# Performance work log

Hardware: AMD Instinct MI355X
Metric: run time of the kernel (lower is better)

Reference implementation:

```python
import jax, jax.numpy as jnp
import numpy as np

N_NODES = 10000
N_EDGES = 640000
IN_CH = 128
HID = 128
OUT = 2


def setup_inputs() -> dict:
    key = jax.random.key(0)
    ks = jax.random.split(key, 12)
    s_in = 1.0 / np.sqrt(IN_CH)
    s_2h = 1.0 / np.sqrt(2 * HID)
    s_h = 1.0 / np.sqrt(HID)
    return {
        "x": jax.random.normal(ks[0], (N_NODES, IN_CH), dtype=jnp.float32),
        "edge_index": jax.random.randint(ks[1], (2, N_EDGES), 0, N_NODES, dtype=jnp.int64),
        # SAGEConv: lin_l applied to aggregated neighbors (has bias), lin_r to self (no bias)
        "W_l": jax.random.uniform(ks[2], (IN_CH, HID), jnp.float32, -s_in, s_in),
        "b_l": jax.random.uniform(ks[3], (HID,), jnp.float32, -s_in, s_in),
        "W_r": jax.random.uniform(ks[4], (IN_CH, HID), jnp.float32, -s_in, s_in),
        # lin0: in -> hid
        "W0": jax.random.uniform(ks[5], (IN_CH, HID), jnp.float32, -s_in, s_in),
        "b0": jax.random.uniform(ks[6], (HID,), jnp.float32, -s_in, s_in),
        # lin1: 2*hid -> hid
        "W1": jax.random.uniform(ks[7], (2 * HID, HID), jnp.float32, -s_2h, s_2h),
        "b1": jax.random.uniform(ks[8], (HID,), jnp.float32, -s_2h, s_2h),
        # lin2: hid -> out
        "W2": jax.random.uniform(ks[9], (HID, OUT), jnp.float32, -s_h, s_h),
        "b2": jax.random.uniform(ks[10], (OUT,), jnp.float32, -s_h, s_h),
    }


def reference(x, edge_index, W_l, b_l, W_r, W0, b0, W1, b1, W2, b2):
    src, dst = edge_index[0], edge_index[1]
    # SAGE mean aggregation: gather source features, scatter-mean onto dst nodes
    msgs = x[src]                                                # [E, in]
    agg = jax.ops.segment_sum(msgs, dst, num_segments=N_NODES)  # [N, in]
    deg = jax.ops.segment_sum(jnp.ones((src.shape[0],), x.dtype), dst,
                              num_segments=N_NODES)              # [N]
    agg = agg / jnp.maximum(deg, 1.0)[:, None]
    # SAGEConv output: lin_l(agg) + lin_r(x)
    h = agg @ W_l + b_l + x @ W_r                                # [N, hid]
    h = jax.nn.relu(h)
    h = jnp.max(h, axis=-2)                                      # [hid] global max pool over nodes
    # concat branch: news node is x[0]
    news = jax.nn.relu(x[0] @ W0 + b0)                           # [hid]
    h = jax.nn.relu(jnp.concatenate([news, h], axis=-1) @ W1 + b1)
    return h @ W2 + b2                                           # [out]
```

## Files before the change

kernel.cpp:

```cpp
#include <hip/hip_runtime.h>
#include <hip/hip_bf16.h>

#define NCH 128
#define NPART 256
#define NRANGE 512
#define SEGCAP 24
#define SEGSTR 32
#define RCAP 2560
#define PSMAX 32

typedef __attribute__((ext_vector_type(8))) short bfrag;
typedef __attribute__((ext_vector_type(4))) float ffrag;
typedef __attribute__((ext_vector_type(2))) float f32x2;

__device__ inline unsigned int f2bf_pair(float lo, float hi) {
    unsigned int ul = __float_as_uint(lo);
    unsigned int uh = __float_as_uint(hi);
    ul = (ul + 0x7fffu + ((ul >> 16) & 1u)) >> 16;
    uh = (uh + 0x7fffu + ((uh >> 16) & 1u)) & 0xffff0000u;
    return (ul & 0xffffu) | uh;
}

__device__ inline void gchunk16(const unsigned short* scsr, int base, int i,
                                const unsigned int* __restrict__ xqU, int lq,
                                int half, float& a0, float& a1, float& a2,
                                float& a3) {
    int s[16]; unsigned int u[16];
#pragma unroll
    for (int j = 0; j < 16; ++j) s[j] = scsr[base + i + 2 * j + half];
#pragma unroll
    for (int j = 0; j < 16; ++j) u[j] = xqU[s[j] * 32 + lq];
#pragma unroll
    for (int j = 0; j < 16; ++j) {
        f32x2 v0 = __builtin_amdgcn_cvt_pk_f32_fp8(u[j], false);
        f32x2 v1 = __builtin_amdgcn_cvt_pk_f32_fp8(u[j], true);
        a0 += v0.x; a1 += v0.y; a2 += v1.x; a3 += v1.y;
    }
}

__device__ inline void gchunk16x2(const unsigned short* scsr, int b1, int i1,
                                  int b2, int i2,
                                  const unsigned int* __restrict__ xqU, int lq,
                                  int half, float& p0, float& p1, float& p2,
                                  float& p3, float& q0, float& q1, float& q2,
                                  float& q3) {
    int sA[16], sB[16]; unsigned int uA[16], uB[16];
#pragma unroll
    for (int j = 0; j < 16; ++j) sA[j] = scsr[b1 + i1 + 2 * j + half];
#pragma unroll
    for (int j = 0; j < 16; ++j) sB[j] = scsr[b2 + i2 + 2 * j + half];
#pragma unroll
    for (int j = 0; j < 16; ++j) uA[j] = xqU[sA[j] * 32 + lq];
#pragma unroll
    for (int j = 0; j < 16; ++j) uB[j] = xqU[sB[j] * 32 + lq];
#pragma unroll
    for (int j = 0; j < 16; ++j) {
        f32x2 v0 = __builtin_amdgcn_cvt_pk_f32_fp8(uA[j], false);
        f32x2 v1 = __builtin_amdgcn_cvt_pk_f32_fp8(uA[j], true);
        p0 += v0.x; p1 += v0.y; p2 += v1.x; p3 += v1.y;
        f32x2 w0 = __builtin_amdgcn_cvt_pk_f32_fp8(uB[j], false);
        f32x2 w1 = __builtin_amdgcn_cvt_pk_f32_fp8(uB[j], true);
        q0 += w0.x; q1 += w0.y; q2 += w1.x; q3 += w1.y;
    }
}

__device__ inline void gtail(const unsigned short* scsr, int base, int i, int d,
                             const unsigned int* __restrict__ xqU, int lq,
                             int half, float& a0, float& a1, float& a2,
                             float& a3) {
    int s[16]; unsigned int u[16];
#pragma unroll
    for (int j = 0; j < 16; ++j) {
        int idx = i + 2 * j + half;
        s[j] = scsr[base + min(idx, d - 1)];
    }
#pragma unroll
    for (int j = 0; j < 16; ++j) u[j] = xqU[s[j] * 32 + lq];
#pragma unroll
    for (int j = 0; j < 16; ++j) {
        int idx = i + 2 * j + half;
        if (idx < d) {
            f32x2 v0 = __builtin_amdgcn_cvt_pk_f32_fp8(u[j], false);
            f32x2 v1 = __builtin_amdgcn_cvt_pk_f32_fp8(u[j], true);
            a0 += v0.x; a1 += v0.y; a2 += v1.x; a3 += v1.y;
        }
    }
}

__global__ __launch_bounds__(512) void k_partprep(
    const float4* __restrict__ x4, const float* __restrict__ Wl,
    const float* __restrict__ Wr, const int* __restrict__ ei32,
    const long long* __restrict__ ei64, unsigned int* __restrict__ M32,
    unsigned int* __restrict__ Wt32, unsigned int* __restrict__ xqU,
    unsigned int* __restrict__ seg, unsigned int* __restrict__ hmaxU,
    int* __restrict__ done, int nq, int N, int E, int PSr, unsigned int Mdiv) {
    const int t = threadIdx.x;
    if (blockIdx.x < NPART) {
        if (blockIdx.x == 0) {
            if (t < 128) hmaxU[t] = 0u;
            if (t == 128) *done = 0;
        }
        __shared__ int sflag;
        __shared__ int cur[NRANGE];
        if (t < 64) {
            int v = ei32[2 * t + 1];
            unsigned long long b = __ballot(v != 0);
            if (t == 0) sflag = (b == 0ULL) ? 1 : 0;
        }
        for (int i = t; i < NRANGE; i += 512) cur[i] = 0;
        __syncthreads();
        const int flag = sflag;
        const int b = blockIdx.x;
        const int ES = (E + NPART - 1) / NPART;
        const int e0 = b * ES, e1 = min(E, e0 + ES);
        for (int bb = e0; bb < e1; bb += 2048) {
            int ebase = bb + t * 4;
            int m = min(4, e1 - ebase);
            if (m <= 0) continue;
            int src4[4], dst4[4];
            if (m == 4) {
                if (flag) {
                    const int4* ps = (const int4*)(ei64 + ebase);
                    const int4* pd = (const int4*)(ei64 + (size_t)E + ebase);
                    int4 q0 = ps[0], q1 = ps[1];
                    int4 r0 = pd[0], r1 = pd[1];
                    src4[0] = q0.x; src4[1] = q0.z; src4[2] = q1.x; src4[3] = q1.z;
                    dst4[0] = r0.x; dst4[1] = r0.z; dst4[2] = r1.x; dst4[3] = r1.z;
                } else {
                    int4 q = *(const int4*)(ei32 + ebase);
                    int4 r0 = *(const int4*)(ei32 + (size_t)E + ebase);
                    src4[0] = q.x; src4[1] = q.y; src4[2] = q.z; src4[3] = q.w;
                    dst4[0] = r0.x; dst4[1] = r0.y; dst4[2] = r0.z; dst4[3] = r0.w;
                }
            } else {
#pragma unroll
                for (int j = 0; j < 4; ++j) {
                    if (j < m) {
                        if (flag) {
                            src4[j] = (int)ei64[ebase + j];
                            dst4[j] = (int)ei64[(size_t)E + ebase + j];
                        } else {
                            src4[j] = ei32[ebase + j];
                            dst4[j] = ei32[(size_t)E + ebase + j];
                        }
                    }
                }
            }
#pragma unroll
            for (int j = 0; j < 4; ++j) {
                if (j < m) {
                    int dstj = dst4[j];
                    int r = Mdiv ? (int)__umulhi((unsigned int)dstj, Mdiv) : dstj;
                    int dl = dstj - r * PSr;
                    int pos = atomicAdd(&cur[r], 1);
                    if (pos < SEGCAP)
                        seg[((size_t)b * NRANGE + r) * SEGSTR + 1 + pos] =
                            ((unsigned int)dl << 16) | (unsigned int)src4[j];
                }
            }
        }
        __syncthreads();
        for (int i = t; i < NRANGE; i += 512)
            seg[((size_t)b * NRANGE + i) * SEGSTR] =
                (unsigned int)min(cur[i], SEGCAP);
        return;
    }
    int i = (int)(blockIdx.x - NPART) * 512 + t;
    if (i < nq) {
        float4 v = x4[i];
        int n = i >> 5, cq = i & 31;
        unsigned int p0 = f2bf_pair(v.x, v.y);
        unsigned int p1 = f2bf_pair(v.z, v.w);
        *(uint2*)(M32 + (size_t)n * 128 + 64 + 2 * cq) = make_uint2(p0, p1);
        unsigned int q = __builtin_amdgcn_cvt_pk_fp8_f32(v.x, v.y, 0u, false);
        q = __builtin_amdgcn_cvt_pk_fp8_f32(v.z, v.w, q, true);
        xqU[(size_t)n * 32 + cq] = q;
        return;
    }
    int j = i - nq;
    if (j < 128 * 128) {
        int c = j & 127, kp = j >> 7;
        int k0 = 2 * kp, k1 = 2 * kp + 1;
        float v0 = (k0 < 128) ? Wl[k0 * 128 + c] : Wr[(k0 - 128) * 128 + c];
        float v1 = (k1 < 128) ? Wl[k1 * 128 + c] : Wr[(k1 - 128) * 128 + c];
        Wt32[c * 128 + kp] = f2bf_pair(v0, v1);
    }
}

__global__ __launch_bounds__(512) void k_aggdense(
    const unsigned int* __restrict__ seg, const unsigned int* __restrict__ M32,
    const unsigned short* __restrict__ xq, const short* __restrict__ Wt,
    const float* __restrict__ bl, unsigned int* __restrict__ hmaxU,
    int* __restrict__ done, const float* __restrict__ x,
    const float* __restrict__ W0, const float* __restrict__ b0,
    const float* __restrict__ W1, const float* __restrict__ b1,
    const float* __restrict__ W2, const float* __restrict__ b2,
    float* __restrict__ out, int N, int PSr) {
    __shared__ unsigned short scsr[RCAP];
    __shared__ unsigned int aggL[PSMAX * 66];
    __shared__ int hist[PSMAX], startp[PSMAX], cur[PSMAX];
    __shared__ float red[8][32];
    __shared__ float hs[1280];
    __shared__ int lastflag;
    const int r = blockIdx.x;
    const int t = threadIdx.x;
    const int wave = t >> 6, lane = t & 63;

    int mycnt = 0;
    uint4 e0 = make_uint4(0, 0, 0, 0), e1 = make_uint4(0, 0, 0, 0),
          e2 = make_uint4(0, 0, 0, 0), e3 = make_uint4(0, 0, 0, 0),
          e4 = make_uint4(0, 0, 0, 0), e5 = make_uint4(0, 0, 0, 0),
          e6 = make_uint4(0, 0, 0, 0);
    if (t < NPART) {
        const uint4* sp = (const uint4*)(seg + ((size_t)t * NRANGE + r) * SEGSTR);
        e0 = sp[0]; e1 = sp[1];
        mycnt = min((int)e0.x, SEGCAP);
        if (mycnt > 7)  e2 = sp[2];
        if (mycnt > 11) e3 = sp[3];
        if (mycnt > 15) e4 = sp[4];
        if (mycnt > 19) e5 = sp[5];
        if (mycnt > 23) e6 = sp[6];
    }

    for (int i = t; i < PSMAX * 66; i += 512) aggL[i] = 0;
    if (t < PSMAX) hist[t] = 0;
    __syncthreads();

#define HIST4(ev, kk)                                                          \
    {                                                                          \
        if ((kk) * 4 + 0 >= 1 && (kk) * 4 + 0 <= mycnt)                        \
            atomicAdd(&hist[(ev).x >> 16], 1);                                 \
        if ((kk) * 4 + 1 <= mycnt) atomicAdd(&hist[(ev).y >> 16], 1);          \
        if ((kk) * 4 + 2 <= mycnt) atomicAdd(&hist[(ev).z >> 16], 1);          \
        if ((kk) * 4 + 3 <= mycnt) atomicAdd(&hist[(ev).w >> 16], 1);          \
    }
    HIST4(e0, 0) HIST4(e1, 1) HIST4(e2, 2) HIST4(e3, 3)
    HIST4(e4, 4) HIST4(e5, 5) HIST4(e6, 6)
#undef HIST4
    __syncthreads();
    if (t < PSMAX) {
        int h = hist[t];
        int ip = h;
#pragma unroll
        for (int off = 1; off < PSMAX; off <<= 1) {
            int u = __shfl_up(ip, off);
            if (lane >= off) ip += u;
        }
        startp[t] = ip - h;
        cur[t] = ip - h;
    }
    __syncthreads();
#define SCAT4(ev, kk)                                                          \
    {                                                                          \
        if ((kk) * 4 + 0 >= 1 && (kk) * 4 + 0 <= mycnt) {                      \
            int p_ = atomicAdd(&cur[(ev).x >> 16], 1);                         \
            if (p_ < RCAP) scsr[p_] = (unsigned short)((ev).x & 0xffffu);      \
        }                                                                      \
        if ((kk) * 4 + 1 <= mycnt) {                                           \
            int p_ = atomicAdd(&cur[(ev).y >> 16], 1);                         \
            if (p_ < RCAP) scsr[p_] = (unsigned short)((ev).y & 0xffffu);      \
        }                                                                      \
        if ((kk) * 4 + 2 <= mycnt) {                                           \
            int p_ = atomicAdd(&cur[(ev).z >> 16], 1);                         \
            if (p_ < RCAP) scsr[p_] = (unsigned short)((ev).z & 0xffffu);      \
        }                                                                      \
        if ((kk) * 4 + 3 <= mycnt) {                                           \
            int p_ = atomicAdd(&cur[(ev).w >> 16], 1);                         \
            if (p_ < RCAP) scsr[p_] = (unsigned short)((ev).w & 0xffffu);      \
        }                                                                      \
    }
    SCAT4(e0, 0) SCAT4(e1, 1) SCAT4(e2, 2) SCAT4(e3, 3)
    SCAT4(e4, 4) SCAT4(e5, 5) SCAT4(e6, 6)
#undef SCAT4
    __syncthreads();

    const int l16 = lane & 15, quad = lane >> 4;
    const int rt = wave & 1, cg = wave >> 1;
    const int lrow = rt * 16 + l16;
    bfrag a[8];
    {
        int mc = min(r * PSr + lrow, N - 1);
#pragma unroll
        for (int kk = 0; kk < 4; ++kk)
            a[4 + kk] = *(const bfrag*)((const short*)(M32 + (size_t)mc * 128 + 64)
                                        + kk * 32 + quad * 8);
    }

    const unsigned int* __restrict__ xqU = (const unsigned int*)xq;
    const int half = lane >> 5, lq = lane & 31;
    const int H = (PSr + 1) >> 1;
    for (int li = wave; li < H; li += 8) {
        int n1 = r * PSr + li;
        if (n1 >= N) break;
        int lj = li + H;
        bool v2 = (lj < PSr) && (r * PSr + lj < N);
        int b1 = startp[li], d1 = hist[li];
        int b2 = v2 ? startp[lj] : 0, d2 = v2 ? hist[lj] : 0;
        float p0 = 0.f, p1 = 0.f, p2 = 0.f, p3 = 0.f;
        float q0 = 0.f, q1 = 0.f, q2 = 0.f, q3 = 0.f;
        int i1 = 0, i2 = 0;
        for (; i1 + 32 <= d1 && i2 + 32 <= d2; i1 += 32, i2 += 32)
            gchunk16x2(scsr, b1, i1, b2, i2, xqU, lq, half,
                       p0, p1, p2, p3, q0, q1, q2, q3);
        for (; i1 + 32 <= d1; i1 += 32)
            gchunk16(scsr, b1, i1, xqU, lq, half, p0, p1, p2, p3);
        for (; i2 + 32 <= d2; i2 += 32)
            gchunk16(scsr, b2, i2, xqU, lq, half, q0, q1, q2, q3);
        if (i1 < d1) gtail(scsr, b1, i1, d1, xqU, lq, half, p0, p1, p2, p3);
        if (i2 < d2) gtail(scsr, b2, i2, d2, xqU, lq, half, q0, q1, q2, q3);
        p0 += __shfl_xor(p0, 32); p1 += __shfl_xor(p1, 32);
        p2 += __shfl_xor(p2, 32); p3 += __shfl_xor(p3, 32);
        q0 += __shfl_xor(q0, 32); q1 += __shfl_xor(q1, 32);
        q2 += __shfl_xor(q2, 32); q3 += __shfl_xor(q3, 32);
        float s1 = 1.0f / fmaxf((float)d1, 1.0f);
        float s2 = 1.0f / fmaxf((float)d2, 1.0f);
        if (half == 0) {
            aggL[li * 66 + 2 * lq]     = f2bf_pair(p0 * s1, p1 * s1);
            aggL[li * 66 + 2 * lq + 1] = f2bf_pair(p2 * s1, p3 * s1);
            if (v2) {
                aggL[lj * 66 + 2 * lq]     = f2bf_pair(q0 * s2, q1 * s2);
                aggL[lj * 66 + 2 * lq + 1] = f2bf_pair(q2 * s2, q3 * s2);
            }
        }
    }
    __syncthreads();

#pragma unroll
    for (int kk = 0; kk < 4; ++kk)
        a[kk] = *(const bfrag*)((const short*)(aggL + lrow * 66 + kk * 16 + quad * 4));
    float mx[2];
#pragma unroll
    for (int ct = 0; ct < 2; ++ct) {
        int col = cg * 32 + ct * 16 + l16;
        float bv = bl[col];
        ffrag acc = {bv, bv, bv, bv};
        const short* wp = Wt + (size_t)col * 256 + quad * 8;
#pragma unroll
        for (int kk = 0; kk < 8; ++kk) {
            bfrag b = *(const bfrag*)(wp + kk * 32);
            acc = __builtin_amdgcn_mfma_f32_16x16x32_bf16(a[kk], b, acc, 0, 0, 0);
        }
        float lm = 0.f;
#pragma unroll
        for (int rr = 0; rr < 4; ++rr) {
            int lr = rt * 16 + quad * 4 + rr;
            int nd = r * PSr + lr;
            if (lr < PSr && nd < N) lm = fmaxf(lm, fmaxf(acc[rr], 0.f));
        }
        lm = fmaxf(lm, __shfl_xor(lm, 16));
        lm = fmaxf(lm, __shfl_xor(lm, 32));
        mx[ct] = lm;
    }
    if (lane < 16) {
        red[wave][l16]      = mx[0];
        red[wave][16 + l16] = mx[1];
    }
    __syncthreads();
    if (t < 128) {
        int cg2 = t >> 5, wi = t & 31;
        float v = fmaxf(red[2 * cg2][wi], red[2 * cg2 + 1][wi]);
        atomicMax(&hmaxU[t], __float_as_uint(v));
    }

    __syncthreads();
    if (t == 0) {
        __threadfence();
        int old = atomicAdd(done, 1);
        lastflag = (old == NRANGE - 1) ? 1 : 0;
    }
    __syncthreads();
    if (!lastflag) return;
    __threadfence();

    float* cat  = hs;
    float* part = hs + 256;
    float* h1p  = hs + 768;
    float* pr   = hs + 896;
    float* xsp  = hs + 1152;
    const int c = t & 127, sg = t >> 7;
    if (t < 128) {
        xsp[t] = x[t];
        cat[128 + t] = __uint_as_float(atomicOr(&hmaxU[t], 0u));
    }
    __syncthreads();
    {
        float a0 = 0.f, a1 = 0.f, a2 = 0.f, a3 = 0.f;
        int k0 = sg * 32;
#pragma unroll
        for (int j = 0; j < 32; j += 4) {
            a0 += xsp[k0 + j + 0] * W0[(k0 + j + 0) * NCH + c];
            a1 += xsp[k0 + j + 1] * W0[(k0 + j + 1) * NCH + c];
            a2 += xsp[k0 + j + 2] * W0[(k0 + j + 2) * NCH + c];
            a3 += xsp[k0 + j + 3] * W0[(k0 + j + 3) * NCH + c];
        }
        part[sg * 128 + c] = (a0 + a1) + (a2 + a3);
    }
    __syncthreads();
    if (t < 128)
        cat[t] = fmaxf(b0[t] + part[t] + part[128 + t] + part[256 + t] + part[384 + t], 0.f);
    __syncthreads();
    {
        float a0 = 0.f, a1 = 0.f, a2 = 0.f, a3 = 0.f;
        int k0 = sg * 64;
#pragma unroll
        for (int j = 0; j < 64; j += 4) {
            a0 += cat[k0 + j + 0] * W1[(k0 + j + 0) * NCH + c];
            a1 += cat[k0 + j + 1] * W1[(k0 + j + 1) * NCH + c];
            a2 += cat[k0 + j + 2] * W1[(k0 + j + 2) * NCH + c];
            a3 += cat[k0 + j + 3] * W1[(k0 + j + 3) * NCH + c];
        }
        part[sg * 128 + c] = (a0 + a1) + (a2 + a3);
    }
    __syncthreads();
    if (t < 128)
        h1p[t] = fmaxf(b1[t] + part[t] + part[128 + t] + part[256 + t] + part[384 + t], 0.f);
    __syncthreads();
    if (t < 128) {
        float2 w = ((const float2*)W2)[t];
        pr[t]       = h1p[t] * w.x;
        pr[128 + t] = h1p[t] * w.y;
    }
    __syncthreads();
    for (int off = 64; off >= 1; off >>= 1) {
        if (t < off) { pr[t] += pr[t + off]; pr[128 + t] += pr[128 + t + off]; }
        __syncthreads();
    }
    if (t == 0) out[0] = pr[0] + b2[0];
    if (t == 1) out[1] = pr[128] + b2[1];
}

__global__ void k_detect(const int* __restrict__ ei, int* __restrict__ flag) {
    int v = ei[2 * threadIdx.x + 1];
    unsigned long long b = __ballot(v != 0);
    if (threadIdx.x == 0) *flag = (b == 0ULL) ? 1 : 0;
}
__global__ void k_hist(const int* __restrict__ ei32, const long long* __restrict__ ei64,
                       const int* __restrict__ flag, int* __restrict__ cnt, int E) {
    int e = blockIdx.x * blockDim.x + threadIdx.x;
    if (e >= E) return;
    int dst = (*flag) ? (int)ei64[(size_t)E + e] : ei32[(size_t)E + e];
    atomicAdd(&cnt[dst], 1);
}
__global__ void k_scan(const int* __restrict__ cnt, int* __restrict__ row_start, int N) {
    __shared__ int lds[1024];
    int t = threadIdx.x;
    int chunk = (N + 1023) / 1024;
    int base = t * chunk;
    int sum = 0;
    for (int i = 0; i < chunk; ++i) {
        int idx = base + i;
        if (idx < N) sum += cnt[idx];
    }
    lds[t] = sum;
    __syncthreads();
    for (int off = 1; off < 1024; off <<= 1) {
        int v = (t >= off) ? lds[t - off] : 0;
        __syncthreads();
        lds[t] += v;
        __syncthreads();
    }
    int run = (t == 0) ? 0 : lds[t - 1];
    for (int i = 0; i < chunk; ++i) {
        int idx = base + i;
        if (idx < N) { row_start[idx] = run; run += cnt[idx]; }
    }
    if (t == 1023) row_start[N] = run;
}
__global__ void k_fill(const int* __restrict__ ei32, const long long* __restrict__ ei64,
                       const int* __restrict__ flag, const int* __restrict__ row_start,
                       int* __restrict__ cursor, int* __restrict__ csr, int E) {
    int e = blockIdx.x * blockDim.x + threadIdx.x;
    if (e >= E) return;
    int src, dst;
    if (*flag) { src = (int)ei64[e]; dst = (int)ei64[(size_t)E + e]; }
    else       { src = ei32[e];      dst = ei32[(size_t)E + e]; }
    int pos = atomicAdd(&cursor[dst], 1);
    csr[row_start[dst] + pos] = src;
}
__global__ __launch_bounds__(256) void k_agg_linmax(
    const float* __restrict__ x, const int* __restrict__ row_start,
    const int* __restrict__ csr, const float* __restrict__ Wl,
    const float* __restrict__ bl, const float* __restrict__ Wr,
    unsigned int* __restrict__ hmaxU, int N, int E) {
    const int lane = threadIdx.x & 63;
    const int wave = threadIdx.x >> 6;
    const int group = blockIdx.x * 4 + wave;
    const int ngroups = (N + 3) / 4;
    const float2* __restrict__ x2  = (const float2*)x;
    const float2* __restrict__ Wl2 = (const float2*)Wl;
    const float2* __restrict__ Wr2 = (const float2*)Wr;
    const float2* __restrict__ bl2 = (const float2*)bl;
    float2 m = make_float2(0.f, 0.f);
    if (group < ngroups) {
        int n0 = group * 4;
        int s[4], d[4];
#pragma unroll
        for (int q = 0; q < 4; ++q) {
            int n = n0 + q;
            if (n < N) { s[q] = row_start[n]; d[q] = row_start[n + 1] - s[q]; }
            else       { s[q] = 0; d[q] = 0; }
        }
        int maxd = max(max(d[0], d[1]), max(d[2], d[3]));
        float2 acc[4];
#pragma unroll
        for (int q = 0; q < 4; ++q) acc[q] = make_float2(0.f, 0.f);
        int idxv[4] = {0, 0, 0, 0};
        for (int i = 0; i < maxd; ++i) {
            int t = i & 63;
            if (t == 0) {
#pragma unroll
                for (int q = 0; q < 4; ++q) {
                    if (i < d[q]) {
                        int a = s[q] + i + lane;
                        a = (a < E) ? a : (E - 1);
                        idxv[q] = csr[a];
                    }
                }
            }
#pragma unroll
            for (int q = 0; q < 4; ++q) {
                if (i < d[q]) {
                    int src = __shfl(idxv[q], t);
                    float2 v = x2[src * 64 + lane];
                    acc[q].x += v.x; acc[q].y += v.y;
                }
            }
        }
        float2 xv[4];
#pragma unroll
        for (int q = 0; q < 4; ++q) {
            float sc = 1.0f / fmaxf((float)d[q], 1.0f);
            acc[q].x *= sc; acc[q].y *= sc;
            int n = n0 + q;
            xv[q] = (n < N) ? x2[n * 64 + lane] : make_float2(0.f, 0.f);
        }
        float2 o[4];
#pragma unroll
        for (int q = 0; q < 4; ++q) o[q] = bl2[lane];
        for (int j = 0; j < 64; ++j) {
            float2 wl0 = Wl2[(2 * j) * 64 + lane];
            float2 wl1 = Wl2[(2 * j + 1) * 64 + lane];
            float2 wr0 = Wr2[(2 * j) * 64 + lane];
            float2 wr1 = Wr2[(2 * j + 1) * 64 + lane];
#pragma unroll
            for (int q = 0; q < 4; ++q) {
                float ax = __shfl(acc[q].x, j);
                float ay = __shfl(acc[q].y, j);
                float xx = __shfl(xv[q].x, j);
                float xy = __shfl(xv[q].y, j);
                o[q].x += ax * wl0.x + ay * wl1.x + xx * wr0.x + xy * wr1.x;
                o[q].y += ax * wl0.y + ay * wl1.y + xx * wr0.y + xy * wr1.y;
            }
        }
#pragma unroll
        for (int q = 0; q < 4; ++q) {
            if (n0 + q < N) {
                m.x = fmaxf(m.x, fmaxf(o[q].x, 0.f));
                m.y = fmaxf(m.y, fmaxf(o[q].y, 0.f));
            }
        }
    }
    __shared__ float2 red2[4][64];
    red2[wave][lane] = m;
    __syncthreads();
    if (wave == 0) {
#pragma unroll
        for (int ww = 1; ww < 4; ++ww) {
            m.x = fmaxf(m.x, red2[ww][lane].x);
            m.y = fmaxf(m.y, red2[ww][lane].y);
        }
        atomicMax(&hmaxU[2 * lane],     __float_as_uint(m.x));
        atomicMax(&hmaxU[2 * lane + 1], __float_as_uint(m.y));
    }
}
__global__ void k_head_fb(const float* __restrict__ x, const float* __restrict__ hmax,
                          const float* __restrict__ W0, const float* __restrict__ b0,
                          const float* __restrict__ W1, const float* __restrict__ b1,
                          const float* __restrict__ W2, const float* __restrict__ b2,
                          float* __restrict__ out) {
    __shared__ float s_cat[2 * NCH];
    __shared__ float s_part[256];
    __shared__ float s_h1[NCH];
    int t = threadIdx.x;
    if (t < NCH) {
        float acc = b0[t];
        for (int k = 0; k < NCH; ++k) acc += x[k] * W0[k * NCH + t];
        s_cat[t] = fmaxf(acc, 0.f);
        s_cat[NCH + t] = hmax[t];
    }
    __syncthreads();
    {
        int c = t & 127, half = t >> 7;
        float p = 0.f;
        int k0 = half * NCH;
        for (int k = k0; k < k0 + NCH; ++k) p += s_cat[k] * W1[k * NCH + c];
        s_part[t] = p;
    }
    __syncthreads();
    if (t < NCH) s_h1[t] = fmaxf(s_part[t] + s_part[NCH + t] + b1[t], 0.f);
    __syncthreads();
    if (t < 2) {
        float o = b2[t];
        for (int k = 0; k < NCH; ++k) o += s_h1[k] * W2[k * 2 + t];
        out[t] = o;
    }
}

extern "C" void kernel_launch(void* const* d_in, const int* in_sizes, int n_in,
                              void* d_out, int out_size, void* d_ws, size_t ws_size,
                              hipStream_t stream) {
    const float* x  = (const float*)d_in[0];
    const void*  ei = d_in[1];
    const float* Wl = (const float*)d_in[2];
    const float* bl = (const float*)d_in[3];
    const float* Wr = (const float*)d_in[4];
    const float* W0 = (const float*)d_in[5];
    const float* b0 = (const float*)d_in[6];
    const float* W1 = (const float*)d_in[7];
    const float* b1 = (const float*)d_in[8];
    const float* W2 = (const float*)d_in[9];
    const float* b2 = (const float*)d_in[10];
    float* out = (float*)d_out;

    const int N = in_sizes[0] / NCH;
    const int E = in_sizes[1] / 2;
    const int nq = N * 32;
    const int PSr = (N + NRANGE - 1) / NRANGE;

    int* iws = (int*)d_ws;
    unsigned int* hmaxU = (unsigned int*)iws;
    int* done = iws + 128;
    unsigned int* seg = (unsigned int*)(iws + 192);
    unsigned int* Wt32 = seg + (size_t)NPART * NRANGE * SEGSTR;
    unsigned int* M32  = Wt32 + 128 * 128;
    unsigned short* xq = (unsigned short*)(M32 + (size_t)N * 128);
    size_t need = ((size_t)192 + (size_t)NPART * NRANGE * SEGSTR + 128 * 128 +
                   (size_t)N * 128 + (size_t)N * 32) * 4;
    bool main_ok = (need <= ws_size) && (N <= NRANGE * PSMAX) && (N <= 65535) &&
                   (PSr >= 1) && (PSr <= PSMAX);

    if (main_ok) {
        unsigned int Mdiv = (PSr > 1)
            ? (unsigned int)(0x100000000ULL / (unsigned long long)PSr + 1ULL)
            : 0u;
        int prepb = (nq + 128 * 128 + 511) / 512;
        k_partprep<<<NPART + prepb, 512, 0, stream>>>(
            (const float4*)x, Wl, Wr, (const int*)ei, (const long long*)ei,
            M32, Wt32, (unsigned int*)xq, seg, hmaxU, done, nq, N, E,
            PSr, Mdiv);
        k_aggdense<<<NRANGE, 512, 0, stream>>>(seg, M32, xq,
                                               (const short*)Wt32,
                                               bl, hmaxU, done, x,
                                               W0, b0, W1, b1, W2, b2, out, N, PSr);
        return;
    }

    int* fcnt      = iws;
    int* fcursor   = iws + N;
    unsigned int* fhmax = (unsigned int*)(iws + 2 * N);
    int* flag      = iws + 2 * N + 128;
    int* frs       = iws + 2 * N + 132;
    int* fcsr      = iws + 3 * N + 144;

    hipMemsetAsync(d_ws, 0, (size_t)(2 * N + 128) * sizeof(int), stream);
    k_detect<<<1, 64, 0, stream>>>((const int*)ei, flag);
    k_hist<<<(E + 255) / 256, 256, 0, stream>>>((const int*)ei, (const long long*)ei,
                                                flag, fcnt, E);
    k_scan<<<1, 1024, 0, stream>>>(fcnt, frs, N);
    k_fill<<<(E + 255) / 256, 256, 0, stream>>>((const int*)ei, (const long long*)ei,
                                                flag, frs, fcursor, fcsr, E);
    int ngroups = (N + 3) / 4;
    k_agg_linmax<<<(ngroups + 3) / 4, 256, 0, stream>>>(x, frs, fcsr, Wl, bl, Wr,
                                                        fhmax, N, E);
    k_head_fb<<<1, 256, 0, stream>>>(x, (const float*)fhmax, W0, b0, W1, b1, W2, b2, out);
}
```

Baseline: 129.3 us.

## Replace atomic last-block reduction with separate head kernel and transpose segment layout

Replaces the global atomicMax plus done-counter last-block pattern with a per-block colmax array and a separate single-block head kernel that reduces it and runs the MLP. Transposes the segment buffer layout so each aggregation block reads contiguous per-range data. Loads the first four segment vectors unconditionally, and drops the two-node-interleaved gather in favour of a simpler one-node-per-wave loop. This trades an extra kernel launch and a colmax round trip for removing threadfence/atomic serialisation, but may lose the memory-level parallelism of the paired gathers.

New measurement: 133.2 us. +3.0%, slower.

```diff
diff --git a/kernel.cpp b/kernel.cpp
--- a/kernel.cpp
+++ b/kernel.cpp
@@ -38,32 +38,6 @@
     }
 }
 
-__device__ inline void gchunk16x2(const unsigned short* scsr, int b1, int i1,
-                                  int b2, int i2,
-                                  const unsigned int* __restrict__ xqU, int lq,
-                                  int half, float& p0, float& p1, float& p2,
-                                  float& p3, float& q0, float& q1, float& q2,
-                                  float& q3) {
-    int sA[16], sB[16]; unsigned int uA[16], uB[16];
-#pragma unroll
-    for (int j = 0; j < 16; ++j) sA[j] = scsr[b1 + i1 + 2 * j + half];
-#pragma unroll
-    for (int j = 0; j < 16; ++j) sB[j] = scsr[b2 + i2 + 2 * j + half];
-#pragma unroll
-    for (int j = 0; j < 16; ++j) uA[j] = xqU[sA[j] * 32 + lq];
-#pragma unroll
-    for (int j = 0; j < 16; ++j) uB[j] = xqU[sB[j] * 32 + lq];
-#pragma unroll
-    for (int j = 0; j < 16; ++j) {
-        f32x2 v0 = __builtin_amdgcn_cvt_pk_f32_fp8(uA[j], false);
-        f32x2 v1 = __builtin_amdgcn_cvt_pk_f32_fp8(uA[j], true);
-        p0 += v0.x; p1 += v0.y; p2 += v1.x; p3 += v1.y;
-        f32x2 w0 = __builtin_amdgcn_cvt_pk_f32_fp8(uB[j], false);
-        f32x2 w1 = __builtin_amdgcn_cvt_pk_f32_fp8(uB[j], true);
-        q0 += w0.x; q1 += w0.y; q2 += w1.x; q3 += w1.y;
-    }
-}
-
 __device__ inline void gtail(const unsigned short* scsr, int base, int i, int d,
                              const unsigned int* __restrict__ xqU, int lq,
                              int half, float& a0, float& a1, float& a2,
@@ -92,14 +66,10 @@
     const float* __restrict__ Wr, const int* __restrict__ ei32,
     const long long* __restrict__ ei64, unsigned int* __restrict__ M32,
     unsigned int* __restrict__ Wt32, unsigned int* __restrict__ xqU,
-    unsigned int* __restrict__ seg, unsigned int* __restrict__ hmaxU,
-    int* __restrict__ done, int nq, int N, int E, int PSr, unsigned int Mdiv) {
+    unsigned int* __restrict__ seg, int nq, int N, int E, int PSr,
+    unsigned int Mdiv) {
     const int t = threadIdx.x;
     if (blockIdx.x < NPART) {
-        if (blockIdx.x == 0) {
-            if (t < 128) hmaxU[t] = 0u;
-            if (t == 128) *done = 0;
-        }
         __shared__ int sflag;
         __shared__ int cur[NRANGE];
         if (t < 64) {
@@ -154,14 +124,14 @@
                     int dl = dstj - r * PSr;
                     int pos = atomicAdd(&cur[r], 1);
                     if (pos < SEGCAP)
-                        seg[((size_t)b * NRANGE + r) * SEGSTR + 1 + pos] =
+                        seg[((size_t)r * NPART + b) * SEGSTR + 1 + pos] =
                             ((unsigned int)dl << 16) | (unsigned int)src4[j];
                 }
             }
         }
         __syncthreads();
         for (int i = t; i < NRANGE; i += 512)
-            seg[((size_t)b * NRANGE + i) * SEGSTR] =
+            seg[((size_t)i * NPART + b) * SEGSTR] =
                 (unsigned int)min(cur[i], SEGCAP);
         return;
     }
@@ -190,18 +160,11 @@
 __global__ __launch_bounds__(512) void k_aggdense(
     const unsigned int* __restrict__ seg, const unsigned int* __restrict__ M32,
     const unsigned short* __restrict__ xq, const short* __restrict__ Wt,
-    const float* __restrict__ bl, unsigned int* __restrict__ hmaxU,
-    int* __restrict__ done, const float* __restrict__ x,
-    const float* __restrict__ W0, const float* __restrict__ b0,
-    const float* __restrict__ W1, const float* __restrict__ b1,
-    const float* __restrict__ W2, const float* __restrict__ b2,
-    float* __restrict__ out, int N, int PSr) {
+    const float* __restrict__ bl, float* __restrict__ colmax, int N, int PSr) {
     __shared__ unsigned short scsr[RCAP];
     __shared__ unsigned int aggL[PSMAX * 66];
     __shared__ int hist[PSMAX], startp[PSMAX], cur[PSMAX];
     __shared__ float red[8][32];
-    __shared__ float hs[1280];
-    __shared__ int lastflag;
     const int r = blockIdx.x;
     const int t = threadIdx.x;
     const int wave = t >> 6, lane = t & 63;
@@ -212,14 +175,14 @@
           e4 = make_uint4(0, 0, 0, 0), e5 = make_uint4(0, 0, 0, 0),
           e6 = make_uint4(0, 0, 0, 0);
     if (t < NPART) {
-        const uint4* sp = (const uint4*)(seg + ((size_t)t * NRANGE + r) * SEGSTR);
-        e0 = sp[0]; e1 = sp[1];
+        const uint4* sp = (const uint4*)(seg + ((size_t)r * NPART + t) * SEGSTR);
+        e0 = sp[0]; e1 = sp[1]; e2 = sp[2]; e3 = sp[3];
         mycnt = min((int)e0.x, SEGCAP);
-        if (mycnt > 7)  e2 = sp[2];
-        if (mycnt > 11) e3 = sp[3];
-        if (mycnt > 15) e4 = sp[4];
-        if (mycnt > 19) e5 = sp[5];
-        if (mycnt > 23) e6 = sp[6];
+        if (mycnt > 15) {
+            e4 = sp[4];
+            if (mycnt > 19) e5 = sp[5];
+            if (mycnt > 23) e6 = sp[6];
+        }
     }
 
     for (int i = t; i < PSMAX * 66; i += 512) aggL[i] = 0;
@@ -288,39 +251,24 @@
 
     const unsigned int* __restrict__ xqU = (const unsigned int*)xq;
     const int half = lane >> 5, lq = lane & 31;
-    const int H = (PSr + 1) >> 1;
-    for (int li = wave; li < H; li += 8) {
-        int n1 = r * PSr + li;
-        if (n1 >= N) break;
-        int lj = li + H;
-        bool v2 = (lj < PSr) && (r * PSr + lj < N);
-        int b1 = startp[li], d1 = hist[li];
-        int b2 = v2 ? startp[lj] : 0, d2 = v2 ? hist[lj] : 0;
-        float p0 = 0.f, p1 = 0.f, p2 = 0.f, p3 = 0.f;
-        float q0 = 0.f, q1 = 0.f, q2 = 0.f, q3 = 0.f;
-        int i1 = 0, i2 = 0;
-        for (; i1 + 32 <= d1 && i2 + 32 <= d2; i1 += 32, i2 += 32)
-            gchunk16x2(scsr, b1, i1, b2, i2, xqU, lq, half,
-                       p0, p1, p2, p3, q0, q1, q2, q3);
-        for (; i1 + 32 <= d1; i1 += 32)
-            gchunk16(scsr, b1, i1, xqU, lq, half, p0, p1, p2, p3);
-        for (; i2 + 32 <= d2; i2 += 32)
-            gchunk16(scsr, b2, i2, xqU, lq, half, q0, q1, q2, q3);
-        if (i1 < d1) gtail(scsr, b1, i1, d1, xqU, lq, half, p0, p1, p2, p3);
-        if (i2 < d2) gtail(scsr, b2, i2, d2, xqU, lq, half, q0, q1, q2, q3);
-        p0 += __shfl_xor(p0, 32); p1 += __shfl_xor(p1, 32);
-        p2 += __shfl_xor(p2, 32); p3 += __shfl_xor(p3, 32);
-        q0 += __shfl_xor(q0, 32); q1 += __shfl_xor(q1, 32);
-        q2 += __shfl_xor(q2, 32); q3 += __shfl_xor(q3, 32);
-        float s1 = 1.0f / fmaxf((float)d1, 1.0f);
-        float s2 = 1.0f / fmaxf((float)d2, 1.0f);
+    for (int li = wave; li < PSr; li += 8) {
+        int node = r * PSr + li;
+        if (node >= N) break;
+        int base = startp[li], d = hist[li];
+        float a0 = 0.f, a1 = 0.f, a2 = 0.f, a3 = 0.f;
+        int i = 0;
+        for (; i + 32 <= d; i += 32)
+            gchunk16(scsr, base, i, xqU, lq, half, a0, a1, a2, a3);
+        if (i < d)
+            gtail(scsr, base, i, d, xqU, lq, half, a0, a1, a2, a3);
+        a0 += __shfl_xor(a0, 32);
+        a1 += __shfl_xor(a1, 32);
+        a2 += __shfl_xor(a2, 32);
+        a3 += __shfl_xor(a3, 32);
+        float sca = 1.0f / fmaxf((float)d, 1.0f);
         if (half == 0) {
-            aggL[li * 66 + 2 * lq]     = f2bf_pair(p0 * s1, p1 * s1);
-            aggL[li * 66 + 2 * lq + 1] = f2bf_pair(p2 * s1, p3 * s1);
-            if (v2) {
-                aggL[lj * 66 + 2 * lq]     = f2bf_pair(q0 * s2, q1 * s2);
-                aggL[lj * 66 + 2 * lq + 1] = f2bf_pair(q2 * s2, q3 * s2);
-            }
+            aggL[li * 66 + 2 * lq]     = f2bf_pair(a0 * sca, a1 * sca);
+            aggL[li * 66 + 2 * lq + 1] = f2bf_pair(a2 * sca, a3 * sca);
         }
     }
     __syncthreads();
@@ -358,29 +306,36 @@
     __syncthreads();
     if (t < 128) {
         int cg2 = t >> 5, wi = t & 31;
-        float v = fmaxf(red[2 * cg2][wi], red[2 * cg2 + 1][wi]);
-        atomicMax(&hmaxU[t], __float_as_uint(v));
-    }
-
-    __syncthreads();
-    if (t == 0) {
-        __threadfence();
-        int old = atomicAdd(done, 1);
-        lastflag = (old == NRANGE - 1) ? 1 : 0;
-    }
-    __syncthreads();
-    if (!lastflag) return;
-    __threadfence();
-
+        colmax[r * 128 + t] = fmaxf(red[2 * cg2][wi], red[2 * cg2 + 1][wi]);
+    }
+}
+
+__global__ __launch_bounds__(512) void k_head(
+    const float* __restrict__ colmax, const float* __restrict__ x,
+    const float* __restrict__ W0, const float* __restrict__ b0,
+    const float* __restrict__ W1, const float* __restrict__ b1,
+    const float* __restrict__ W2, const float* __restrict__ b2,
+    float* __restrict__ out) {
+    __shared__ float hs[1280];
     float* cat  = hs;
     float* part = hs + 256;
     float* h1p  = hs + 768;
     float* pr   = hs + 896;
     float* xsp  = hs + 1152;
+    const int t = threadIdx.x;
     const int c = t & 127, sg = t >> 7;
+    {
+        float m = 0.f;
+        const float* p = colmax + sg * 128 + c;
+#pragma unroll 8
+        for (int rr = 0; rr < NRANGE / 4; ++rr) m = fmaxf(m, p[rr * 512]);
+        part[sg * 128 + c] = m;
+    }
+    __syncthreads();
     if (t < 128) {
         xsp[t] = x[t];
-        cat[128 + t] = __uint_as_float(atomicOr(&hmaxU[t], 0u));
+        cat[128 + t] = fmaxf(fmaxf(part[t], part[128 + t]),
+                             fmaxf(part[256 + t], part[384 + t]));
     }
     __syncthreads();
     {
@@ -628,14 +583,13 @@
     const int PSr = (N + NRANGE - 1) / NRANGE;
 
     int* iws = (int*)d_ws;
-    unsigned int* hmaxU = (unsigned int*)iws;
-    int* done = iws + 128;
-    unsigned int* seg = (unsigned int*)(iws + 192);
+    float* colmax = (float*)iws;
+    unsigned int* seg = (unsigned int*)(iws + NRANGE * 128);
     unsigned int* Wt32 = seg + (size_t)NPART * NRANGE * SEGSTR;
     unsigned int* M32  = Wt32 + 128 * 128;
     unsigned short* xq = (unsigned short*)(M32 + (size_t)N * 128);
-    size_t need = ((size_t)192 + (size_t)NPART * NRANGE * SEGSTR + 128 * 128 +
-                   (size_t)N * 128 + (size_t)N * 32) * 4;
+    size_t need = ((size_t)NRANGE * 128 + (size_t)NPART * NRANGE * SEGSTR +
+                   128 * 128 + (size_t)N * 128 + (size_t)N * 32) * 4;
     bool main_ok = (need <= ws_size) && (N <= NRANGE * PSMAX) && (N <= 65535) &&
                    (PSr >= 1) && (PSr <= PSMAX);
 
@@ -646,12 +600,11 @@
         int prepb = (nq + 128 * 128 + 511) / 512;
         k_partprep<<<NPART + prepb, 512, 0, stream>>>(
             (const float4*)x, Wl, Wr, (const int*)ei, (const long long*)ei,
-            M32, Wt32, (unsigned int*)xq, seg, hmaxU, done, nq, N, E,
-            PSr, Mdiv);
+            M32, Wt32, (unsigned int*)xq, seg, nq, N, E, PSr, Mdiv);
         k_aggdense<<<NRANGE, 512, 0, stream>>>(seg, M32, xq,
                                                (const short*)Wt32,
-                                               bl, hmaxU, done, x,
-                                               W0, b0, W1, b1, W2, b2, out, N, PSr);
+                                               bl, colmax, N, PSr);
+        k_head<<<1, 512, 0, stream>>>(colmax, x, W0, b0, W1, b1, W2, b2, out);
         return;
     }
 
```
